# Performance work log

Measured on AMD Instinct MI355X. Metric: run time of the kernel, lower is better.

The kernel has to match this reference:

```python
import jax, jax.numpy as jnp
import numpy as np

B, N, S, K = 32, 2048, 64, 128   # clouds, pts/cloud, fps centers (ratio=64/2048), max neighbors
R = 0.2                          # radius ball-query
SLOPE = 0.2                      # LeakyReLU negative slope
C_CONV = [3, 64, 128, 512]       # PointConv local nn
D_FEAT = 512


def leaky(x):
    return jnp.where(x >= 0, x, SLOPE * x)


def _init_linear(key, din, dout):
    kw, kb = jax.random.split(key)
    lim = 1.0 / np.sqrt(din)
    W = jax.random.uniform(kw, (din, dout), minval=-lim, maxval=lim, dtype=jnp.float32)
    b = jax.random.uniform(kb, (dout,), minval=-lim, maxval=lim, dtype=jnp.float32)
    return W, b


def setup_inputs() -> dict:
    key = jax.random.key(0)
    ks = jax.random.split(key, 6)
    pos = jax.random.uniform(ks[0], (B * N, 3), dtype=jnp.float32)
    batch = (jnp.arange(B * N, dtype=jnp.int32) // N)
    W1, b1 = _init_linear(ks[1], 3, 64)
    W2, b2 = _init_linear(ks[2], 64, 128)
    W3, b3 = _init_linear(ks[3], 128, 512)
    W4, b4 = _init_linear(ks[4], D_FEAT + 3, 512)
    W5, b5 = _init_linear(ks[5], 512, 1024)
    return {"pos": pos, "batch": batch,
            "W1": W1, "b1": b1, "W2": W2, "b2": b2, "W3": W3, "b3": b3,
            "W4": W4, "b4": b4, "W5": W5, "b5": b5}


def _fps_one(p):
    """Deterministic farthest point sampling on one cloud p:[N,3] -> idx:[S]."""
    d0 = jnp.sum((p - p[0]) ** 2, axis=-1)

    def step(dists, _):
        nxt = jnp.argmax(dists).astype(jnp.int32)
        dists = jnp.minimum(dists, jnp.sum((p - p[nxt]) ** 2, axis=-1))
        return dists, nxt

    _, rest = jax.lax.scan(step, d0, None, length=S - 1)
    return jnp.concatenate([jnp.zeros((1,), jnp.int32), rest])


def _encoder(pos, W1, b1, W2, b2, W3, b3, W4, b4, W5, b5):
    pts = pos.reshape(B, N, 3)
    idx = jax.vmap(_fps_one)(pts)                                   # [B,S] local fps indices
    centers = jnp.take_along_axis(pts, idx[:, :, None], axis=1)     # [B,S,3]

    # radius ball query (first-by-index up to K neighbors, like torch_cluster cap)
    d2 = jnp.sum((centers[:, :, None, :] - pts[:, None, :, :]) ** 2, axis=-1)  # [B,S,N]
    inball = d2 < R * R
    keys = jnp.where(inball, jnp.arange(N, dtype=jnp.int32)[None, None, :], N)
    nbr = jnp.sort(keys, axis=-1)[:, :, :K]                          # [B,S,K]
    valid = nbr < N
    nbr = jnp.where(valid, nbr, 0)

    # PointConv: gather relative positions -> MLP -> masked max aggregation
    nbr_pos = jnp.take_along_axis(pts[:, None, :, :], nbr[..., None], axis=2)  # [B,S,K,3]
    rel = nbr_pos - centers[:, :, None, :]
    h = leaky(rel @ W1 + b1)
    h = leaky(h @ W2 + b2)
    h = leaky(h @ W3 + b3)                                           # [B,S,K,512]
    h = jnp.where(valid[..., None], h, -jnp.inf)
    feat = jnp.max(h, axis=2)                                        # [B,S,512] (self always in ball)

    g = jnp.concatenate([feat, centers], axis=-1).reshape(B * S, D_FEAT + 3)
    g = leaky(g @ W4 + b4)
    out = g @ W5 + b5                                                # [B*S,1024]
    mean, logvar = out[:, :512], out[:, 512:]
    std = jnp.exp(0.5 * logvar)

    # global edge indices (x_idx = neighbor point id, y_idx = center id), -1 padded
    x_idx = jnp.where(valid, nbr + jnp.arange(B, dtype=jnp.int32)[:, None, None] * N, -1).reshape(-1)
    y_idx = jnp.where(valid, jnp.arange(B * S, dtype=jnp.int32).reshape(B, S, 1), -1).reshape(-1)
    return mean, std, x_idx, y_idx


def reference(pos, batch, W1, b1, W2, b2, W3, b3, W4, b4, W5, b5):
    # batch is implied by the fixed [B,N] layout (sorted, equal-size clouds)
    return _encoder(pos, W1, b1, W2, b2, W3, b3, W4, b4, W5, b5)
```

## Files before the change

kernel.cpp:

```cpp
#include <hip/hip_runtime.h>
#include <hip/hip_bf16.h>

#define NB 32
#define NP 2048
#define NS 64
#define NK 128

#define MEAN_OFF 0
#define STD_OFF  1048576
#define XIDX_OFF 2097152
#define YIDX_OFF 2359296

#define GA_LD 576

typedef __attribute__((ext_vector_type(4)))  short s4;
typedef __attribute__((ext_vector_type(8)))  short short8;
typedef __attribute__((ext_vector_type(16))) float f32x16;

static __device__ __forceinline__ float leaky(float x){ return x >= 0.0f ? x : 0.2f * x; }

static __device__ __forceinline__ unsigned short bf16u(float v){
    __hip_bfloat16 h = __float2bfloat16(v);
    return *(unsigned short*)&h;
}

static __device__ __forceinline__ float d2s(float ax,float ay,float az,float bx,float by,float bz){
    float dx = __fsub_rn(ax,bx), dy = __fsub_rn(ay,by), dz = __fsub_rn(az,bz);
    return __fadd_rn(__fadd_rn(__fmul_rn(dx,dx),__fmul_rn(dy,dy)),__fmul_rn(dz,dz));
}

__global__ __launch_bounds__(256) void fps_prep_kernel(const float* __restrict__ pos,
                                                       float* __restrict__ centersWs,
                                                       const float* __restrict__ W2,
                                                       const float* __restrict__ W3,
                                                       const float* __restrict__ W4,
                                                       const float* __restrict__ W5,
                                                       __hip_bfloat16* __restrict__ W2T,
                                                       __hip_bfloat16* __restrict__ W3T,
                                                       __hip_bfloat16* __restrict__ W4T,
                                                       __hip_bfloat16* __restrict__ W5T)
{
    if (blockIdx.x >= NB) {
        int g = (blockIdx.x - NB)*256 + threadIdx.x;
        if (g < 65536) {
            int c = g >> 7, i = g & 127;
            int byte = c*256 + ((i*2) ^ ((c&15)<<4));
            W3T[byte>>1] = __float2bfloat16(W3[(size_t)i*512 + c]);
        }
        if (g < 8192) {
            int i = g >> 6, j = g & 63;
            W2T[g] = __float2bfloat16(W2[(size_t)j*128 + i]);
        }
        for (int e = g; e < 512*GA_LD; e += 131072) {
            int n = e / GA_LD, k = e - n*GA_LD;
            float v = (k < 515) ? W4[(size_t)k*512 + n] : 0.0f;
            W4T[e] = __float2bfloat16(v);
        }
        for (int e = g; e < 1024*512; e += 131072) {
            int n = e >> 9, k = e & 511;
            W5T[e] = __float2bfloat16(W5[(size_t)k*1024 + n]);
        }
        return;
    }

    int b = blockIdx.x;
    int t = threadIdx.x;
    __shared__ float px[NP], py[NP], pz[NP];
    __shared__ float redv[2][4];
    __shared__ int   redi[2][4];

    const float* pb = pos + (size_t)b * NP * 3;
    for (int n = t; n < NP; n += 256) {
        px[n] = pb[n*3+0]; py[n] = pb[n*3+1]; pz[n] = pb[n*3+2];
    }
    __syncthreads();

    float p0x = px[0], p0y = py[0], p0z = pz[0];
    float dl[8];
    #pragma unroll
    for (int q = 0; q < 8; q++) {
        int n = t + q*256;
        dl[q] = d2s(px[n],py[n],pz[n], p0x,p0y,p0z);
    }
    if (t == 0) {
        centersWs[(b*NS)*3+0] = p0x;
        centersWs[(b*NS)*3+1] = p0y;
        centersWs[(b*NS)*3+2] = p0z;
    }

    int w = t >> 6;
    for (int s = 1; s < NS; s++) {
        float bv = -1.0f; int bi = 0;
        #pragma unroll
        for (int q = 0; q < 8; q++) {
            int n = t + q*256;
            if (dl[q] > bv) { bv = dl[q]; bi = n; }
        }
        #pragma unroll
        for (int m = 32; m > 0; m >>= 1) {
            float ov = __shfl_xor(bv, m);
            int   oi = __shfl_xor(bi, m);
            if (ov > bv || (ov == bv && oi < bi)) { bv = ov; bi = oi; }
        }
        if ((t & 63) == 0) { redv[s&1][w] = bv; redi[s&1][w] = bi; }
        __syncthreads();
        float v = redv[s&1][0]; int j = redi[s&1][0];
        #pragma unroll
        for (int k = 1; k < 4; k++) {
            if (redv[s&1][k] > v || (redv[s&1][k] == v && redi[s&1][k] < j)) { v = redv[s&1][k]; j = redi[s&1][k]; }
        }
        float cx = px[j], cy = py[j], cz = pz[j];
        if (t == 0) {
            centersWs[(b*NS+s)*3+0] = cx;
            centersWs[(b*NS+s)*3+1] = cy;
            centersWs[(b*NS+s)*3+2] = cz;
        }
        #pragma unroll
        for (int q = 0; q < 8; q++) {
            int n = t + q*256;
            dl[q] = fminf(dl[q], d2s(px[n],py[n],pz[n], cx,cy,cz));
        }
    }
}

__global__ __launch_bounds__(256, 3) void ball_mlp_kernel(
    const float* __restrict__ pos,
    const float* __restrict__ W1, const float* __restrict__ b1,
    const float* __restrict__ b2, const float* __restrict__ b3,
    const __hip_bfloat16* __restrict__ W2Tp,
    const __hip_bfloat16* __restrict__ W3Tp,
    const float* __restrict__ centersWs,
    float* __restrict__ out,
    __hip_bfloat16* __restrict__ gAb)
{
    __shared__ char smem[53776];
    char*  h1s  = smem;
    char*  h2s  = smem + 16384;
    float* relL = (float*)(smem + 49152);
    int*   nbL  = (int*)(smem + 49152);
    float* b2s  = (float*)(smem + 51200);
    int*   cntW4= (int*)(smem + 51712);
    float* b3s  = (float*)(smem + 51728);
    float* red  = (float*)(smem + 32768);

    const short* W2T  = (const short*)W2Tp;
    const char*  W3Tb = (const char*)W3Tp;

    int r = blockIdx.x, b = r >> 6, tid = threadIdx.x;
    int l = tid & 63, w = tid >> 6;
    int l31 = l & 31;
    int hsel = l >> 5;
    int jsel8 = hsel * 8;
    int colsel = hsel * 16;

    float cx = centersWs[r*3+0], cy = centersWs[r*3+1], cz = centersWs[r*3+2];

    int wi = w & 1, wk = w >> 1;
    short8 aW[2][4];
    #pragma unroll
    for (int rt = 0; rt < 2; rt++) {
        int ia = (2*wi + rt)*32 + l31;
        #pragma unroll
        for (int ks = 0; ks < 4; ks++)
            aW[rt][ks] = *(const short8*)(W2T + ia*64 + ks*16 + jsel8);
    }

    const float* pb = pos + (size_t)b * NP * 3;
    {
        int myCnt = 0;
        #pragma unroll
        for (int c = 0; c < 8; c++) {
            int n = w*512 + c*64 + l;
            float x = pb[n*3+0], y = pb[n*3+1], z = pb[n*3+2];
            bool in = d2s(cx,cy,cz, x,y,z) < 0.04f;
            unsigned long long m = __ballot(in);
            int before = __popcll(m & ((1ull << l) - 1ull));
            int p = myCnt + before;
            if (in && p < NK) nbL[w*NK + p] = n;
            myCnt += (int)__popcll(m);
        }
        if (l == 0) cntW4[w] = myCnt;
    }
    b3s[tid] = b3[tid];
    b3s[tid + 256] = b3[tid + 256];
    __syncthreads();

    int c0 = cntW4[0], c1 = cntW4[1], c2 = cntW4[2], c3 = cntW4[3];
    int cnt = c0 + c1 + c2 + c3;
    cnt = cnt > NK ? NK : cnt;

    int nv = 0;
    if (tid < NK) {
        bool valid = tid < cnt;
        int seg = 0, off = 0;
        if (tid >= c0)           { seg = 1; off = c0; }
        if (tid >= c0 + c1)      { seg = 2; off = c0 + c1; }
        if (tid >= c0 + c1 + c2) { seg = 3; off = c0 + c1 + c2; }
        if (valid) nv = nbL[seg*NK + (tid - off)];
        out[XIDX_OFF + r*NK + tid] = valid ? (float)(nv + b*NP) : -1.0f;
        out[YIDX_OFF + r*NK + tid] = valid ? (float)r : -1.0f;
    }
    __syncthreads();

    if (tid < NK) {
        const float* pp = pb + (size_t)nv*3;
        relL[tid*4+0] = pp[0] - cx;
        relL[tid*4+1] = pp[1] - cy;
        relL[tid*4+2] = pp[2] - cz;
        relL[tid*4+3] = 0.0f;
        b2s[tid] = b2[tid];
    }
    __syncthreads();

    {
        int jg = (tid & 15) * 4;
        float4 w0 = *(const float4*)&W1[jg];
        float4 w1 = *(const float4*)&W1[64 + jg];
        float4 w2 = *(const float4*)&W1[128 + jg];
        float4 bb = *(const float4*)&b1[jg];
        #pragma unroll
        for (int e = 0; e < 8; e++) {
            int k = (tid >> 4) + e*16;
            float4 r4 = *(const float4*)&relL[k*4];
            s4 pk;
            pk[0] = (short)bf16u(leaky(bb.x + r4.x*w0.x + r4.y*w1.x + r4.z*w2.x));
            pk[1] = (short)bf16u(leaky(bb.y + r4.x*w0.y + r4.y*w1.y + r4.z*w2.y));
            pk[2] = (short)bf16u(leaky(bb.z + r4.x*w0.z + r4.y*w1.z + r4.z*w2.z));
            pk[3] = (short)bf16u(leaky(bb.w + r4.x*w0.w + r4.y*w1.w + r4.z*w2.w));
            *(s4*)(h1s + k*128 + ((jg*2) ^ ((k&7)<<4))) = pk;
        }
    }
    __syncthreads();

    {
        f32x16 acc[2][2];
        #pragma unroll
        for (int q = 0; q < 16; q++) { acc[0][0][q]=0.f; acc[0][1][q]=0.f; acc[1][0][q]=0.f; acc[1][1][q]=0.f; }
        int kc0 = (2*wk)*32 + l31, kc1 = kc0 + 32;
        #pragma unroll
        for (int ks = 0; ks < 4; ks++) {
            int bc = ks*32 + colsel;
            short8 bh0 = *(short8*)(h1s + kc0*128 + (bc ^ ((kc0&7)<<4)));
            short8 bh1 = *(short8*)(h1s + kc1*128 + (bc ^ ((kc1&7)<<4)));
            acc[0][0] = __builtin_amdgcn_mfma_f32_32x32x16_bf16(aW[0][ks], bh0, acc[0][0], 0, 0, 0);
            acc[0][1] = __builtin_amdgcn_mfma_f32_32x32x16_bf16(aW[0][ks], bh1, acc[0][1], 0, 0, 0);
            acc[1][0] = __builtin_amdgcn_mfma_f32_32x32x16_bf16(aW[1][ks], bh0, acc[1][0], 0, 0, 0);
            acc[1][1] = __builtin_amdgcn_mfma_f32_32x32x16_bf16(aW[1][ks], bh1, acc[1][1], 0, 0, 0);
        }
        #pragma unroll
        for (int rt = 0; rt < 2; rt++) {
            int ibase = (2*wi + rt)*32 + 4*hsel;
            float4 bias[4];
            #pragma unroll
            for (int g = 0; g < 4; g++) bias[g] = *(const float4*)&b2s[ibase + g*8];
            #pragma unroll
            for (int ct = 0; ct < 2; ct++) {
                int k = (ct == 0) ? kc0 : kc1;
                #pragma unroll
                for (int g = 0; g < 4; g++) {
                    s4 pk;
                    pk[0] = (short)bf16u(leaky(acc[rt][ct][g*4+0] + bias[g].x));
                    pk[1] = (short)bf16u(leaky(acc[rt][ct][g*4+1] + bias[g].y));
                    pk[2] = (short)bf16u(leaky(acc[rt][ct][g*4+2] + bias[g].z));
                    pk[3] = (short)bf16u(leaky(acc[rt][ct][g*4+3] + bias[g].w));
                    *(s4*)(h2s + k*256 + (((ibase + g*8)*2) ^ ((k&15)<<4))) = pk;
                }
            }
        }
    }
    __syncthreads();

    char* buf0 = h1s;
    char* buf1 = h1s + 8192;
    char* buf2 = smem + 16384;
    char* buf3 = smem + 24576;

#define STAGE_W3(CH, DST)                                                                              \
    {                                                                                                  \
        const char* _s = W3Tb + (CH)*8192 + w*2048 + l*16;                                             \
        char* _d = (DST) + w*2048;                                                                     \
        __builtin_amdgcn_global_load_lds((const __attribute__((address_space(1))) void*)(_s),          \
                                         (__attribute__((address_space(3))) void*)(_d), 16, 0, 0);     \
        __builtin_amdgcn_global_load_lds((const __attribute__((address_space(1))) void*)(_s + 1024),   \
                                         (__attribute__((address_space(3))) void*)(_d + 1024), 16, 0, 0); \
    }

    STAGE_W3(0, buf0);
    STAGE_W3(1, buf1);

    short8 a3[8];
    {
        int row = w*32 + l31;
        #pragma unroll
        for (int ks = 0; ks < 8; ks++) {
            int bc = ks*32 + colsel;
            a3[ks] = *(short8*)(h2s + row*256 + (bc ^ ((row&15)<<4)));
        }
    }
    __syncthreads();
    STAGE_W3(2, buf2);

    int kb0 = w*32 + 4*hsel;
    #pragma unroll
    for (int t = 0; t < 16; t++) {
        if (t <= 13)      { asm volatile("s_waitcnt vmcnt(4)" ::: "memory"); }
        else if (t == 14) { asm volatile("s_waitcnt vmcnt(2)" ::: "memory"); }
        else              { asm volatile("s_waitcnt vmcnt(0)" ::: "memory"); }
        __builtin_amdgcn_sched_barrier(0);
        __builtin_amdgcn_s_barrier();
        __builtin_amdgcn_sched_barrier(0);

        if (t + 3 < 16) {
            char* nbuf = ((t+3)&3) == 0 ? buf0 : ((t+3)&3) == 1 ? buf1 : ((t+3)&3) == 2 ? buf2 : buf3;
            STAGE_W3(t+3, nbuf);
        }
        __builtin_amdgcn_sched_barrier(0);

        char* buf = (t&3) == 0 ? buf0 : (t&3) == 1 ? buf1 : (t&3) == 2 ? buf2 : buf3;
        f32x16 acc;
        #pragma unroll
        for (int q = 0; q < 16; q++) acc[q] = 0.f;
        #pragma unroll
        for (int ks = 0; ks < 8; ks++) {
            int bc = ks*32 + colsel;
            short8 bv = *(short8*)(buf + l31*256 + (bc ^ ((l31&15)<<4)));
            acc = __builtin_amdgcn_mfma_f32_32x32x16_bf16(a3[ks], bv, acc, 0, 0, 0);
        }
        float m = -INFINITY;
        #pragma unroll
        for (int reg = 0; reg < 16; reg++) {
            int kloc = (reg&3) + 8*(reg>>2);
            if (kb0 + kloc < cnt) m = fmaxf(m, acc[reg]);
        }
        m = fmaxf(m, __shfl_xor(m, 32));
        if (l < 32) red[w*512 + t*32 + l31] = m;
        __builtin_amdgcn_sched_barrier(0);
    }
    __syncthreads();

    #pragma unroll
    for (int e = 0; e < 2; e++) {
        int c = tid + e*256;
        float m = fmaxf(fmaxf(red[c], red[512 + c]), fmaxf(red[1024 + c], red[1536 + c]));
        gAb[(size_t)r*GA_LD + c] = __float2bfloat16(leaky(m + b3s[c]));
    }
    if (tid < 64) {
        float v = 0.0f;
        if (tid == 0) v = cx; else if (tid == 1) v = cy; else if (tid == 2) v = cz;
        gAb[(size_t)r*GA_LD + 512 + tid] = __float2bfloat16(v);
    }
#undef STAGE_W3
}

__global__ __launch_bounds__(256) void fc1_kernel(const __hip_bfloat16* __restrict__ gAb,
                                                  const __hip_bfloat16* __restrict__ W4T,
                                                  const float* __restrict__ b4,
                                                  __hip_bfloat16* __restrict__ g2b)
{
    __shared__ char smem[16384];
    char* As = smem;
    char* Bs = smem + 8192;

    int bx = blockIdx.x & 7;
    int by = blockIdx.x >> 3;
    int tid = threadIdx.x;
    int l = tid & 63, w = tid >> 6;
    int wm = w & 1, wn = w >> 1;
    int colsel = (l >> 5) * 16;

    f32x16 acc;
    #pragma unroll
    for (int q = 0; q < 16; q++) acc[q] = 0.f;

    int ra = wm*32 + (l & 31);
    int rn = wn*32 + (l & 31);

    for (int kb = 0; kb < GA_LD; kb += 64) {
        #pragma unroll
        for (int it = 0; it < 2; it++) {
            int e = it*256 + tid;
            int row = e >> 3, seg = e & 7;
            short8 va = *(const short8*)(gAb + (size_t)(by*64 + row)*GA_LD + kb + seg*8);
            *(short8*)(As + row*128 + ((seg*16) ^ ((row&7)<<4))) = va;
            short8 vb = *(const short8*)(W4T + (size_t)(bx*64 + row)*GA_LD + kb + seg*8);
            *(short8*)(Bs + row*128 + ((seg*16) ^ ((row&7)<<4))) = vb;
        }
        __syncthreads();
        #pragma unroll
        for (int ks = 0; ks < 4; ks++) {
            int bc = ks*32 + colsel;
            short8 av = *(short8*)(As + ra*128 + (bc ^ ((ra&7)<<4)));
            short8 bv = *(short8*)(Bs + rn*128 + (bc ^ ((rn&7)<<4)));
            acc = __builtin_amdgcn_mfma_f32_32x32x16_bf16(av, bv, acc, 0, 0, 0);
        }
        __syncthreads();
    }

    int col = bx*64 + wn*32 + (l & 31);
    float bcol = b4[col];
    int rbase = by*64 + wm*32 + 4*(l>>5);
    #pragma unroll
    for (int reg = 0; reg < 16; reg++) {
        int row = rbase + (reg&3) + 8*(reg>>2);
        g2b[(size_t)row*512 + col] = __float2bfloat16(leaky(acc[reg] + bcol));
    }
}

__global__ __launch_bounds__(256) void fc2_kernel(const __hip_bfloat16* __restrict__ g2b,
                                                  const __hip_bfloat16* __restrict__ W5T,
                                                  const float* __restrict__ b5,
                                                  float* __restrict__ out)
{
    __shared__ char smem[16384];
    char* As = smem;
    char* Bs = smem + 8192;

    int bx = blockIdx.x & 15;
    int by = blockIdx.x >> 4;
    int tid = threadIdx.x;
    int l = tid & 63, w = tid >> 6;
    int wm = w & 1, wn = w >> 1;
    int colsel = (l >> 5) * 16;

    f32x16 acc;
    #pragma unroll
    for (int q = 0; q < 16; q++) acc[q] = 0.f;

    int ra = wm*32 + (l & 31);
    int rn = wn*32 + (l & 31);

    for (int kb = 0; kb < 512; kb += 64) {
        #pragma unroll
        for (int it = 0; it < 2; it++) {
            int e = it*256 + tid;
            int row = e >> 3, seg = e & 7;
            short8 va = *(const short8*)(g2b + (size_t)(by*64 + row)*512 + kb + seg*8);
            *(short8*)(As + row*128 + ((seg*16) ^ ((row&7)<<4))) = va;
            short8 vb = *(const short8*)(W5T + (size_t)(bx*64 + row)*512 + kb + seg*8);
            *(short8*)(Bs + row*128 + ((seg*16) ^ ((row&7)<<4))) = vb;
        }
        __syncthreads();
        #pragma unroll
        for (int ks = 0; ks < 4; ks++) {
            int bc = ks*32 + colsel;
            short8 av = *(short8*)(As + ra*128 + (bc ^ ((ra&7)<<4)));
            short8 bv = *(short8*)(Bs + rn*128 + (bc ^ ((rn&7)<<4)));
            acc = __builtin_amdgcn_mfma_f32_32x32x16_bf16(av, bv, acc, 0, 0, 0);
        }
        __syncthreads();
    }

    int col = bx*64 + wn*32 + (l & 31);
    float bcol = b5[col];
    int rbase = by*64 + wm*32 + 4*(l>>5);
    #pragma unroll
    for (int reg = 0; reg < 16; reg++) {
        int row = rbase + (reg&3) + 8*(reg>>2);
        float v = acc[reg] + bcol;
        if (col < 512) {
            out[MEAN_OFF + (size_t)row*512 + col] = v;
        } else {
            out[STD_OFF + (size_t)row*512 + (col - 512)] = expf(0.5f*v);
        }
    }
}

extern "C" void kernel_launch(void* const* d_in, const int* in_sizes, int n_in,
                              void* d_out, int out_size, void* d_ws, size_t ws_size,
                              hipStream_t stream) {
    const float* pos = (const float*)d_in[0];
    const float* W1  = (const float*)d_in[2];
    const float* b1  = (const float*)d_in[3];
    const float* W2  = (const float*)d_in[4];
    const float* b2  = (const float*)d_in[5];
    const float* W3  = (const float*)d_in[6];
    const float* b3  = (const float*)d_in[7];
    const float* W4  = (const float*)d_in[8];
    const float* b4  = (const float*)d_in[9];
    const float* W5  = (const float*)d_in[10];
    const float* b5  = (const float*)d_in[11];
    float* out = (float*)d_out;

    char* ws = (char*)d_ws;
    float* centersWs = (float*)(ws);
    __hip_bfloat16* gAb = (__hip_bfloat16*)(ws + 1081344);
    __hip_bfloat16* g2b = (__hip_bfloat16*)(ws + 3440640);
    __hip_bfloat16* W2T = (__hip_bfloat16*)(ws + 5537792);
    __hip_bfloat16* W3T = (__hip_bfloat16*)(ws + 5554176);
    __hip_bfloat16* W4T = (__hip_bfloat16*)(ws + 5685248);
    __hip_bfloat16* W5T = (__hip_bfloat16*)(ws + 6275072);

    hipLaunchKernelGGL(fps_prep_kernel, dim3(NB + 512), dim3(256), 0, stream,
                       pos, centersWs, W2, W3, W4, W5, W2T, W3T, W4T, W5T);
    hipLaunchKernelGGL(ball_mlp_kernel, dim3(NB*NS), dim3(256), 0, stream,
                       pos, W1,b1, b2,b3, W2T, W3T, centersWs, out, gAb);
    hipLaunchKernelGGL(fc1_kernel, dim3(256), dim3(256), 0, stream, gAb, W4T, b4, g2b);
    hipLaunchKernelGGL(fc2_kernel, dim3(512), dim3(256), 0, stream, g2b, W5T, b5, out);
}
```

Before: 163.1 us.

## Keep layer-2 output in registers via permlane swap, shrink LDS for occupancy

Layer 2 of the point MLP is restructured so that each wave computes all 128 output channels for its own 32 neighbours. The results are packed to bf16 with v_cvt_pk_bf16_f32 and rearranged with v_permlane32_swap directly into the A fragments for layer 3, so the h2s shared-memory round trip and one barrier go away. This shrinks LDS from about 53KB to 37KB and raises launch bounds to 4 blocks per CU. W3 staging also starts at kernel entry, overlapping with the ball query, and max reductions are held in registers until the end of the loop. In exchange, W2 fragments are re-read from global or cache on every iteration, and register pressure may be tight at the higher occupancy target.

```diff
diff --git a/kernel.cpp b/kernel.cpp
--- a/kernel.cpp
+++ b/kernel.cpp
@@ -22,6 +22,15 @@
 static __device__ __forceinline__ unsigned short bf16u(float v){
     __hip_bfloat16 h = __float2bfloat16(v);
     return *(unsigned short*)&h;
+}
+
+static __device__ __forceinline__ unsigned cvtpk(float a, float b){
+    unsigned d;
+    asm("v_cvt_pk_bf16_f32 %0, %1, %2" : "=v"(d) : "v"(a), "v"(b));
+    return d;
+}
+static __device__ __forceinline__ void plswap(unsigned &a, unsigned &b){
+    asm volatile("v_permlane32_swap_b32 %0, %1" : "+v"(a), "+v"(b));
 }
 
 static __device__ __forceinline__ float d2s(float ax,float ay,float az,float bx,float by,float bz){
@@ -123,7 +132,7 @@
     }
 }
 
-__global__ __launch_bounds__(256, 3) void ball_mlp_kernel(
+__global__ __launch_bounds__(256, 4) void ball_mlp_kernel(
     const float* __restrict__ pos,
     const float* __restrict__ W1, const float* __restrict__ b1,
     const float* __restrict__ b2, const float* __restrict__ b3,
@@ -133,15 +142,13 @@
     float* __restrict__ out,
     __hip_bfloat16* __restrict__ gAb)
 {
-    __shared__ char smem[53776];
+    __shared__ char smem[37392];
     char*  h1s  = smem;
-    char*  h2s  = smem + 16384;
-    float* relL = (float*)(smem + 49152);
-    int*   nbL  = (int*)(smem + 49152);
-    float* b2s  = (float*)(smem + 51200);
-    int*   cntW4= (int*)(smem + 51712);
-    float* b3s  = (float*)(smem + 51728);
-    float* red  = (float*)(smem + 32768);
+    float* relL = (float*)(smem + 32768);
+    int*   nbL  = (int*)(smem + 32768);
+    float* b2s  = (float*)(smem + 34816);
+    float* b3s  = (float*)(smem + 35328);
+    int*   cntW4= (int*)(smem + 37376);
 
     const short* W2T  = (const short*)W2Tp;
     const char*  W3Tb = (const char*)W3Tp;
@@ -153,17 +160,20 @@
     int jsel8 = hsel * 8;
     int colsel = hsel * 16;
 
+#define STAGE_W3(CH, DST)                                                                              \
+    {                                                                                                  \
+        const char* _s = W3Tb + (CH)*8192 + w*2048 + l*16;                                             \
+        char* _d = (DST) + w*2048;                                                                     \
+        __builtin_amdgcn_global_load_lds((const __attribute__((address_space(1))) void*)(_s),          \
+                                         (__attribute__((address_space(3))) void*)(_d), 16, 0, 0);     \
+        __builtin_amdgcn_global_load_lds((const __attribute__((address_space(1))) void*)(_s + 1024),   \
+                                         (__attribute__((address_space(3))) void*)(_d + 1024), 16, 0, 0); \
+    }
+
+    STAGE_W3(0, smem + 16384);
+    STAGE_W3(1, smem + 24576);
+
     float cx = centersWs[r*3+0], cy = centersWs[r*3+1], cz = centersWs[r*3+2];
-
-    int wi = w & 1, wk = w >> 1;
-    short8 aW[2][4];
-    #pragma unroll
-    for (int rt = 0; rt < 2; rt++) {
-        int ia = (2*wi + rt)*32 + l31;
-        #pragma unroll
-        for (int ks = 0; ks < 4; ks++)
-            aW[rt][ks] = *(const short8*)(W2T + ia*64 + ks*16 + jsel8);
-    }
 
     const float* pb = pos + (size_t)b * NP * 3;
     {
@@ -232,75 +242,57 @@
     }
     __syncthreads();
 
+    short8 a3[8];
     {
-        f32x16 acc[2][2];
-        #pragma unroll
-        for (int q = 0; q < 16; q++) { acc[0][0][q]=0.f; acc[0][1][q]=0.f; acc[1][0][q]=0.f; acc[1][1][q]=0.f; }
-        int kc0 = (2*wk)*32 + l31, kc1 = kc0 + 32;
+        int kcol = w*32 + l31;
+        short8 bh[4];
         #pragma unroll
         for (int ks = 0; ks < 4; ks++) {
             int bc = ks*32 + colsel;
-            short8 bh0 = *(short8*)(h1s + kc0*128 + (bc ^ ((kc0&7)<<4)));
-            short8 bh1 = *(short8*)(h1s + kc1*128 + (bc ^ ((kc1&7)<<4)));
-            acc[0][0] = __builtin_amdgcn_mfma_f32_32x32x16_bf16(aW[0][ks], bh0, acc[0][0], 0, 0, 0);
-            acc[0][1] = __builtin_amdgcn_mfma_f32_32x32x16_bf16(aW[0][ks], bh1, acc[0][1], 0, 0, 0);
-            acc[1][0] = __builtin_amdgcn_mfma_f32_32x32x16_bf16(aW[1][ks], bh0, acc[1][0], 0, 0, 0);
-            acc[1][1] = __builtin_amdgcn_mfma_f32_32x32x16_bf16(aW[1][ks], bh1, acc[1][1], 0, 0, 0);
-        }
-        #pragma unroll
-        for (int rt = 0; rt < 2; rt++) {
-            int ibase = (2*wi + rt)*32 + 4*hsel;
-            float4 bias[4];
+            bh[ks] = *(short8*)(h1s + kcol*128 + (bc ^ ((kcol&7)<<4)));
+        }
+        #pragma unroll
+        for (int it = 0; it < 4; it++) {
+            short8 aWf[4];
             #pragma unroll
-            for (int g = 0; g < 4; g++) bias[g] = *(const float4*)&b2s[ibase + g*8];
+            for (int ks = 0; ks < 4; ks++)
+                aWf[ks] = *(const short8*)(W2T + (it*32 + l31)*64 + ks*16 + jsel8);
+            f32x16 acc;
             #pragma unroll
-            for (int ct = 0; ct < 2; ct++) {
-                int k = (ct == 0) ? kc0 : kc1;
-                #pragma unroll
-                for (int g = 0; g < 4; g++) {
-                    s4 pk;
-                    pk[0] = (short)bf16u(leaky(acc[rt][ct][g*4+0] + bias[g].x));
-                    pk[1] = (short)bf16u(leaky(acc[rt][ct][g*4+1] + bias[g].y));
-                    pk[2] = (short)bf16u(leaky(acc[rt][ct][g*4+2] + bias[g].z));
-                    pk[3] = (short)bf16u(leaky(acc[rt][ct][g*4+3] + bias[g].w));
-                    *(s4*)(h2s + k*256 + (((ibase + g*8)*2) ^ ((k&15)<<4))) = pk;
-                }
+            for (int q = 0; q < 16; q++) acc[q] = 0.f;
+            #pragma unroll
+            for (int ks = 0; ks < 4; ks++)
+                acc = __builtin_amdgcn_mfma_f32_32x32x16_bf16(aWf[ks], bh[ks], acc, 0, 0, 0);
+            int ibase = it*32 + 4*hsel;
+            #pragma unroll
+            for (int g = 0; g < 4; g++) {
+                float4 bb = *(const float4*)&b2s[ibase + g*8];
+                acc[g*4+0] = leaky(acc[g*4+0] + bb.x);
+                acc[g*4+1] = leaky(acc[g*4+1] + bb.y);
+                acc[g*4+2] = leaky(acc[g*4+2] + bb.z);
+                acc[g*4+3] = leaky(acc[g*4+3] + bb.w);
             }
-        }
-    }
-    __syncthreads();
-
-    char* buf0 = h1s;
-    char* buf1 = h1s + 8192;
-    char* buf2 = smem + 16384;
-    char* buf3 = smem + 24576;
-
-#define STAGE_W3(CH, DST)                                                                              \
-    {                                                                                                  \
-        const char* _s = W3Tb + (CH)*8192 + w*2048 + l*16;                                             \
-        char* _d = (DST) + w*2048;                                                                     \
-        __builtin_amdgcn_global_load_lds((const __attribute__((address_space(1))) void*)(_s),          \
-                                         (__attribute__((address_space(3))) void*)(_d), 16, 0, 0);     \
-        __builtin_amdgcn_global_load_lds((const __attribute__((address_space(1))) void*)(_s + 1024),   \
-                                         (__attribute__((address_space(3))) void*)(_d + 1024), 16, 0, 0); \
-    }
-
-    STAGE_W3(0, buf0);
-    STAGE_W3(1, buf1);
-
-    short8 a3[8];
-    {
-        int row = w*32 + l31;
-        #pragma unroll
-        for (int ks = 0; ks < 8; ks++) {
-            int bc = ks*32 + colsel;
-            a3[ks] = *(short8*)(h2s + row*256 + (bc ^ ((row&15)<<4)));
-        }
-    }
-    __syncthreads();
-    STAGE_W3(2, buf2);
+            #pragma unroll
+            for (int hf = 0; hf < 2; hf++) {
+                unsigned A0 = cvtpk(acc[hf*8+0], acc[hf*8+1]);
+                unsigned A1 = cvtpk(acc[hf*8+2], acc[hf*8+3]);
+                unsigned B0 = cvtpk(acc[hf*8+4], acc[hf*8+5]);
+                unsigned B1 = cvtpk(acc[hf*8+6], acc[hf*8+7]);
+                plswap(A0, B0);
+                plswap(A1, B1);
+                union { unsigned u[4]; short8 s; } f;
+                f.u[0] = A0; f.u[1] = A1; f.u[2] = B0; f.u[3] = B1;
+                a3[2*it + hf] = f.s;
+            }
+        }
+    }
+    __syncthreads();
+
+    STAGE_W3(2, smem);
+    STAGE_W3(3, smem + 8192);
 
     int kb0 = w*32 + 4*hsel;
+    float mred[16];
     #pragma unroll
     for (int t = 0; t < 16; t++) {
         if (t <= 13)      { asm volatile("s_waitcnt vmcnt(4)" ::: "memory"); }
@@ -310,13 +302,13 @@
         __builtin_amdgcn_s_barrier();
         __builtin_amdgcn_sched_barrier(0);
 
-        if (t + 3 < 16) {
-            char* nbuf = ((t+3)&3) == 0 ? buf0 : ((t+3)&3) == 1 ? buf1 : ((t+3)&3) == 2 ? buf2 : buf3;
+        if (t >= 1 && t + 3 < 16) {
+            char* nbuf = smem + 8192*((t+1)&3);
             STAGE_W3(t+3, nbuf);
         }
         __builtin_amdgcn_sched_barrier(0);
 
-        char* buf = (t&3) == 0 ? buf0 : (t&3) == 1 ? buf1 : (t&3) == 2 ? buf2 : buf3;
+        char* buf = smem + 8192*((t+2)&3);
         f32x16 acc;
         #pragma unroll
         for (int q = 0; q < 16; q++) acc[q] = 0.f;
@@ -333,15 +325,21 @@
             if (kb0 + kloc < cnt) m = fmaxf(m, acc[reg]);
         }
         m = fmaxf(m, __shfl_xor(m, 32));
-        if (l < 32) red[w*512 + t*32 + l31] = m;
+        mred[t] = m;
         __builtin_amdgcn_sched_barrier(0);
     }
-    __syncthreads();
-
+
+    float* redf = (float*)(smem + 16384);
+    if (l < 32) {
+        #pragma unroll
+        for (int t = 0; t < 16; t++)
+            redf[w*512 + t*32 + l31] = mred[t];
+    }
+    __syncthreads();
     #pragma unroll
     for (int e = 0; e < 2; e++) {
         int c = tid + e*256;
-        float m = fmaxf(fmaxf(red[c], red[512 + c]), fmaxf(red[1024 + c], red[1536 + c]));
+        float m = fmaxf(fmaxf(redf[c], redf[512 + c]), fmaxf(redf[1024 + c], redf[1536 + c]));
         gAb[(size_t)r*GA_LD + c] = __float2bfloat16(leaky(m + b3s[c]));
     }
     if (tid < 64) {
```

Measured after the change: 151.6 us. 7.1% less time.
